# Performance work log

Measured on AMD Instinct MI355X. Metric: run time of the kernel, lower is better.

The kernel has to match this reference:

```python
import jax, jax.numpy as jnp
import numpy as np

B, N, DIM, H = 32, 480, 1024, 16


def setup_inputs() -> dict:
    key = jax.random.key(0)
    ks = jax.random.split(key, 7)
    s = 0.02
    return {
        "q": jax.random.normal(ks[0], (B, N, DIM), jnp.float32),
        "Wq": jax.random.normal(ks[1], (DIM, DIM), jnp.float32) * s,
        "Wk": jax.random.normal(ks[2], (DIM, DIM), jnp.float32) * s,
        "Wv": jax.random.normal(ks[3], (DIM, DIM), jnp.float32) * s,
        "pe": jax.random.normal(ks[4], (480, 480), jnp.float32),
        "Wo": jax.random.normal(ks[5], (DIM, DIM), jnp.float32) * s,
        "bo": jnp.zeros((DIM,), jnp.float32),
    }


def reference(q, Wq, Wk, Wv, pe, Wo, bo):
    b, n, dim = q.shape
    h = H
    d = dim // h
    scale = d ** -0.5
    # self-attention: k = v = q (pre-projection)
    qp = (q @ Wq.T).reshape(b, n, h, d).transpose(0, 2, 1, 3)  # b h n d
    kp = (q @ Wk.T).reshape(b, n, h, d).transpose(0, 2, 1, 3)
    vp = (q @ Wv.T).reshape(b, n, h, d).transpose(0, 2, 1, 3)
    dots = jnp.einsum("bhid,bhjd->bhij", qp, kp) * scale
    dots = dots + pe[:n, :n]  # learned additive positional bias
    attn = jax.nn.softmax(dots, axis=-1)
    out = jnp.einsum("bhij,bhjd->bhid", attn, vp)
    out = out.transpose(0, 2, 1, 3).reshape(b, n, dim)
    return out @ Wo.T + bo
```

## Files before the change

### kernel.cpp

```cpp
#include <hip/hip_runtime.h>
#include <hip/hip_bf16.h>
#include <stdint.h>

#define B_   32
#define N_   480
#define DIM_ 1024
#define H_   16
#define D_   64
#define M_   (B_*N_)
#define BH_  (B_*H_)

typedef __bf16 bf16;
typedef __bf16 bf16x4 __attribute__((ext_vector_type(4)));
typedef __bf16 bf16x8 __attribute__((ext_vector_type(8)));
typedef short  short4v __attribute__((ext_vector_type(4)));
typedef float  f32x4  __attribute__((ext_vector_type(4)));

__device__ __forceinline__ void gld_lds16(const void* g, void* l) {
    using GP = const __attribute__((address_space(1))) unsigned int*;
    using LP = __attribute__((address_space(3))) unsigned int*;
    __builtin_amdgcn_global_load_lds((GP)(uintptr_t)g, (LP)(unsigned int)(uintptr_t)l, 16, 0, 0);
}

__global__ void cvt4(const float* __restrict__ in, bf16* __restrict__ out, int n4) {
    int i = blockIdx.x * 256 + threadIdx.x;
    if (i >= n4) return;
    float4 v = ((const float4*)in)[i];
    bf16x4 o = { (bf16)v.x, (bf16)v.y, (bf16)v.z, (bf16)v.w };
    ((bf16x4*)out)[i] = o;
}

__global__ void cvtW(const float* __restrict__ Wq, const float* __restrict__ Wk,
                     const float* __restrict__ Wv, const float* __restrict__ Wo,
                     bf16* __restrict__ Wcat, bf16* __restrict__ Wob) {
    int i = blockIdx.x * 256 + threadIdx.x;
    const float* src; bf16* dst;
    switch (blockIdx.y) {
        case 0: src = Wq; dst = Wcat;                break;
        case 1: src = Wk; dst = Wcat + DIM_*DIM_;    break;
        case 2: src = Wv; dst = Wcat + 2*DIM_*DIM_;  break;
        default: src = Wo; dst = Wob;                break;
    }
    float4 v = ((const float4*)src)[i];
    bf16x4 o = { (bf16)v.x, (bf16)v.y, (bf16)v.z, (bf16)v.w };
    ((bf16x4*)dst)[i] = o;
}

#define GEMM_PRE()                                                            \
    const int tid  = threadIdx.x;                                             \
    const int lane = tid & 63;                                                \
    const int wid  = tid >> 6;                                                \
    const int wm   = wid & 1, wn = wid >> 1;                                  \
    const int m0   = blockIdx.y * 128;                                        \
    const int n0   = blockIdx.x * 128;                                        \
    const int lm   = lane & 15, lq = lane >> 4;                               \
    const int aLane = (lane >> 3) * 1024 + (((lane & 7) ^ (lane >> 3)) & 7) * 8; \
    const bf16* Asrc = A  + (m0 + wid*32) * 1024 + aLane;                     \
    const bf16* Bsrc = Bw + (n0 + wid*32) * 1024 + aLane;                     \
    bf16* AsDst = As + (wid*32)*64;                                           \
    bf16* BsDst = Bs + (wid*32)*64;                                           \
    int rowA[4], rowB[4];                                                     \
    _Pragma("unroll") for (int m = 0; m < 4; ++m) rowA[m] = (wm*64 + m*16 + lm)*64; \
    _Pragma("unroll") for (int n = 0; n < 4; ++n) rowB[n] = (wn*64 + n*16 + lm)*64; \
    const int sw = lm & 7;                                                    \
    int phys[2];                                                              \
    phys[0] = ((lq)     ^ sw) * 8;                                            \
    phys[1] = ((4 + lq) ^ sw) * 8;

#define GEMM_KLOOP(FIRST, SECOND)                                             \
    for (int k0 = 0; k0 < 1024; k0 += 64) {                                   \
        _Pragma("unroll") for (int j = 0; j < 4; ++j) {                       \
            gld_lds16(Asrc + k0 + j*8192, AsDst + j*512);                     \
            gld_lds16(Bsrc + k0 + j*8192, BsDst + j*512);                     \
        }                                                                     \
        __syncthreads();                                                      \
        _Pragma("unroll") for (int ks = 0; ks < 2; ++ks) {                    \
            bf16x8 af[4], bfr[4];                                             \
            _Pragma("unroll") for (int m = 0; m < 4; ++m)                     \
                af[m]  = *(const bf16x8*)&As[rowA[m] + phys[ks]];             \
            _Pragma("unroll") for (int n = 0; n < 4; ++n)                     \
                bfr[n] = *(const bf16x8*)&Bs[rowB[n] + phys[ks]];             \
            _Pragma("unroll") for (int m = 0; m < 4; ++m)                     \
                _Pragma("unroll") for (int n = 0; n < 4; ++n)                 \
                    acc[m][n] = __builtin_amdgcn_mfma_f32_16x16x32_bf16(      \
                        FIRST, SECOND, acc[m][n], 0, 0, 0);                   \
        }                                                                     \
        __syncthreads();                                                      \
    }

__global__ __launch_bounds__(256) void gemm_qkv(const bf16* __restrict__ A, const bf16* __restrict__ Bw,
                                                bf16* __restrict__ Qp, bf16* __restrict__ Kp,
                                                bf16* __restrict__ Vt) {
    __shared__ bf16 As[128*64];
    __shared__ bf16 Bs[128*64];
    GEMM_PRE();
    const int part = n0 >> 10;
    f32x4 acc[4][4] = {};

    if (part != 2) {
        GEMM_KLOOP(af[m], bfr[n]);
        bf16* dst = (part == 0) ? Qp : Kp;
        int hh[4], dd[4];
#pragma unroll
        for (int n = 0; n < 4; ++n) {
            int rem = (n0 + wn*64 + n*16 + lm) & 1023;
            hh[n] = rem >> 6; dd[n] = rem & 63;
        }
#pragma unroll
        for (int m = 0; m < 4; ++m) {
#pragma unroll
            for (int r = 0; r < 4; ++r) {
                int gm = m0 + wm*64 + m*16 + lq*4 + r;
                int b  = gm / 480;
                int nn = gm - b*480;
#pragma unroll
                for (int n = 0; n < 4; ++n)
                    dst[((b*16 + hh[n])*480 + nn)*64 + dd[n]] = (bf16)acc[m][n][r];
            }
        }
    } else {
        GEMM_KLOOP(bfr[n], af[m]);
#pragma unroll
        for (int m = 0; m < 4; ++m) {
            int gmBase = m0 + wm*64 + m*16;
            int b  = gmBase / 480;
            int nn = gmBase - b*480 + lm;
#pragma unroll
            for (int n = 0; n < 4; ++n)
#pragma unroll
                for (int r = 0; r < 4; ++r) {
                    int rem = (n0 + wn*64 + n*16 + lq*4 + r) & 1023;
                    int h = rem >> 6, d = rem & 63;
                    Vt[((b*16 + h)*64 + d)*480 + nn] = (bf16)acc[m][n][r];
                }
        }
    }
}

#define KT 96
#define KS_LD 72
#define VS_LD 104
__global__ __launch_bounds__(320) void attn(const bf16* __restrict__ Qp, const bf16* __restrict__ Kp,
                                            const bf16* __restrict__ Vt, const float* __restrict__ pe,
                                            bf16* __restrict__ O) {
    __shared__ bf16 Ks[KT*KS_LD];
    __shared__ bf16 Vs[64*VS_LD];
    const int tid  = threadIdx.x;
    const int lane = tid & 63, wid = tid >> 6;
    const int bh   = blockIdx.y;
    const int b    = bh >> 4, h = bh & 15;
    const int qblk = blockIdx.x * 80;
    const int lm   = lane & 15, lq = lane >> 4;
    const int qbase = bh * (N_ * 64);

    bf16x8 qb[2];
#pragma unroll
    for (int ks = 0; ks < 2; ++ks)
        qb[ks] = *(const bf16x8*)&Qp[qbase + (qblk + wid*16 + lm)*64 + ks*32 + lq*8];
    const float* peRow = pe + (qblk + wid*16 + lm)*480;

    f32x4 ot[4] = {};
    float lsum = 0.f;

    for (int kt = 0; kt < 5; ++kt) {
        __syncthreads();
        for (int c = tid; c < 768; c += 320) {
            int row = c >> 3, of = (c & 7) * 8;
            *(uint4*)&Ks[row*KS_LD + of] = *(const uint4*)&Kp[qbase + (kt*KT + row)*64 + of];
        }
        for (int c = tid; c < 768; c += 320) {
            int row = c / 12, of = (c % 12) * 8;
            *(uint4*)&Vs[row*VS_LD + of] = *(const uint4*)&Vt[qbase + row*480 + kt*KT + of];
        }
        __syncthreads();

        short4v pb[6];
#pragma unroll
        for (int mf = 0; mf < 6; ++mf) {
            f32x4 s = {};
#pragma unroll
            for (int ks = 0; ks < 2; ++ks) {
                bf16x8 ka = *(const bf16x8*)&Ks[(mf*16 + lm)*KS_LD + ks*32 + lq*8];
                s = __builtin_amdgcn_mfma_f32_16x16x32_bf16(ka, qb[ks], s, 0, 0, 0);
            }
            bf16x4 pv;
#pragma unroll
            for (int r = 0; r < 4; ++r) {
                float e = __expf(s[r] * 0.125f + peRow[kt*KT + mf*16 + lq*4 + r]);
                lsum += e;
                pv[r] = (bf16)e;
            }
            pb[mf] = __builtin_bit_cast(short4v, pv);
        }

#pragma unroll
        for (int df = 0; df < 4; ++df)
#pragma unroll
            for (int mf = 0; mf < 6; ++mf) {
                short4v va = *(const short4v*)&Vs[(df*16 + lm)*VS_LD + mf*16 + lq*4];
                ot[df] = __builtin_amdgcn_mfma_f32_16x16x16bf16_1k(va, pb[mf], ot[df], 0, 0, 0);
            }
    }

    lsum += __shfl_xor(lsum, 16);
    lsum += __shfl_xor(lsum, 32);
    float rl = 1.f / lsum;

    __syncthreads();
    bf16* Os = Ks;
#pragma unroll
    for (int df = 0; df < 4; ++df)
#pragma unroll
        for (int r = 0; r < 4; ++r)
            Os[(wid*16 + lm)*KS_LD + df*16 + lq*4 + r] = (bf16)(ot[df][r] * rl);
    __syncthreads();
    for (int c = tid; c < 640; c += 320) {
        int row = c >> 3, d0 = (c & 7) * 8;
        uint4 u = *(const uint4*)&Os[row*KS_LD + d0];
        *(uint4*)&O[(b*480 + qblk + row)*1024 + h*64 + d0] = u;
    }
}

__global__ __launch_bounds__(256) void gemm_out(const bf16* __restrict__ A, const bf16* __restrict__ Bw,
                                                const float* __restrict__ bo, float* __restrict__ out) {
    __shared__ bf16 As[128*64];
    __shared__ bf16 Bs[128*64];
    GEMM_PRE();
    f32x4 acc[4][4] = {};
    GEMM_KLOOP(af[m], bfr[n]);
#pragma unroll
    for (int m = 0; m < 4; ++m)
#pragma unroll
        for (int n = 0; n < 4; ++n)
#pragma unroll
            for (int r = 0; r < 4; ++r) {
                int gm = m0 + wm*64 + m*16 + lq*4 + r;
                int gn = n0 + wn*64 + n*16 + lm;
                out[gm*1024 + gn] = acc[m][n][r] + bo[gn];
            }
}

extern "C" void kernel_launch(void* const* d_in, const int* in_sizes, int n_in,
                              void* d_out, int out_size, void* d_ws, size_t ws_size,
                              hipStream_t stream) {
    const float* q  = (const float*)d_in[0];
    const float* Wq = (const float*)d_in[1];
    const float* Wk = (const float*)d_in[2];
    const float* Wv = (const float*)d_in[3];
    const float* pe = (const float*)d_in[4];
    const float* Wo = (const float*)d_in[5];
    const float* bo = (const float*)d_in[6];
    float* out = (float*)d_out;

    char* ws = (char*)d_ws;
    bf16* Abf  = (bf16*)(ws);
    bf16* Wcat = (bf16*)(ws + 31457280);
    bf16* Wob  = (bf16*)(ws + 31457280 + 6291456);
    bf16* Qp   = (bf16*)(ws + 39845888);
    bf16* Kp   = (bf16*)(ws + 71303168);
    bf16* Vt   = (bf16*)(ws + 102760448);

    cvt4<<<(M_*DIM_/4 + 255)/256, 256, 0, stream>>>(q, Abf, M_*DIM_/4);
    cvtW<<<dim3(DIM_*DIM_/4/256, 4), 256, 0, stream>>>(Wq, Wk, Wv, Wo, Wcat, Wob);

    gemm_qkv<<<dim3(24, 120), 256, 0, stream>>>(Abf, Wcat, Qp, Kp, Vt);
    attn<<<dim3(6, 512), 320, 0, stream>>>(Qp, Kp, Vt, pe, Abf);
    gemm_out<<<dim3(8, 120), 256, 0, stream>>>(Abf, Wob, bo, out);
}
```

Baseline: 414.1 us.

## Process two query tiles per wave in attention to reuse K/V LDS reads

Each wave in the attention kernel now handles 32 query rows as two 16-row tiles instead of one. Every K and V fragment read from LDS therefore feeds two MFMAs, and the block count along the query axis is halved. The LDS row pads also shrink and K/V share one buffer, and the output staging now uses vector stores. In exchange, register pressure roughly doubles for the accumulators, occupancy may drop, and the new pads leave rows only 8-byte aligned for the 16-byte LDS accesses.

Result: slower. 457.0 us (+10.4%).

```diff
diff --git a/kernel.cpp b/kernel.cpp
--- a/kernel.cpp
+++ b/kernel.cpp
@@ -138,29 +138,33 @@
 }
 
 #define KT 96
-#define KS_LD 72
-#define VS_LD 104
+#define KS_LD 68
+#define VS_LD 100
 __global__ __launch_bounds__(320) void attn(const bf16* __restrict__ Qp, const bf16* __restrict__ Kp,
                                             const bf16* __restrict__ Vt, const float* __restrict__ pe,
                                             bf16* __restrict__ O) {
-    __shared__ bf16 Ks[KT*KS_LD];
-    __shared__ bf16 Vs[64*VS_LD];
+    __shared__ bf16 Sm[KT*KS_LD + 64*VS_LD];
+    bf16* Ks = Sm;
+    bf16* Vs = Sm + KT*KS_LD;
     const int tid  = threadIdx.x;
     const int lane = tid & 63, wid = tid >> 6;
     const int bh   = blockIdx.y;
     const int b    = bh >> 4, h = bh & 15;
-    const int qblk = blockIdx.x * 80;
+    const int qblk = blockIdx.x * 160;
     const int lm   = lane & 15, lq = lane >> 4;
     const int qbase = bh * (N_ * 64);
 
-    bf16x8 qb[2];
-#pragma unroll
-    for (int ks = 0; ks < 2; ++ks)
-        qb[ks] = *(const bf16x8*)&Qp[qbase + (qblk + wid*16 + lm)*64 + ks*32 + lq*8];
-    const float* peRow = pe + (qblk + wid*16 + lm)*480;
-
-    f32x4 ot[4] = {};
-    float lsum = 0.f;
+    bf16x8 qb[2][2];
+#pragma unroll
+    for (int t = 0; t < 2; ++t)
+#pragma unroll
+        for (int ks = 0; ks < 2; ++ks)
+            qb[t][ks] = *(const bf16x8*)&Qp[qbase + (qblk + wid*32 + t*16 + lm)*64 + ks*32 + lq*8];
+    const float* peA = pe + (qblk + wid*32      + lm)*480;
+    const float* peB = pe + (qblk + wid*32 + 16 + lm)*480;
+
+    f32x4 ot[2][4] = {};
+    float lsum[2] = {0.f, 0.f};
 
     for (int kt = 0; kt < 5; ++kt) {
         __syncthreads();
@@ -174,23 +178,26 @@
         }
         __syncthreads();
 
-        short4v pb[6];
+        short4v pbA[6], pbB[6];
 #pragma unroll
         for (int mf = 0; mf < 6; ++mf) {
-            f32x4 s = {};
+            f32x4 sA = {}, sB = {};
 #pragma unroll
             for (int ks = 0; ks < 2; ++ks) {
                 bf16x8 ka = *(const bf16x8*)&Ks[(mf*16 + lm)*KS_LD + ks*32 + lq*8];
-                s = __builtin_amdgcn_mfma_f32_16x16x32_bf16(ka, qb[ks], s, 0, 0, 0);
-            }
-            bf16x4 pv;
+                sA = __builtin_amdgcn_mfma_f32_16x16x32_bf16(ka, qb[0][ks], sA, 0, 0, 0);
+                sB = __builtin_amdgcn_mfma_f32_16x16x32_bf16(ka, qb[1][ks], sB, 0, 0, 0);
+            }
+            bf16x4 pA, pB;
 #pragma unroll
             for (int r = 0; r < 4; ++r) {
-                float e = __expf(s[r] * 0.125f + peRow[kt*KT + mf*16 + lq*4 + r]);
-                lsum += e;
-                pv[r] = (bf16)e;
-            }
-            pb[mf] = __builtin_bit_cast(short4v, pv);
+                float eA = __expf(sA[r] * 0.125f + peA[kt*KT + mf*16 + lq*4 + r]);
+                float eB = __expf(sB[r] * 0.125f + peB[kt*KT + mf*16 + lq*4 + r]);
+                lsum[0] += eA; lsum[1] += eB;
+                pA[r] = (bf16)eA; pB[r] = (bf16)eB;
+            }
+            pbA[mf] = __builtin_bit_cast(short4v, pA);
+            pbB[mf] = __builtin_bit_cast(short4v, pB);
         }
 
 #pragma unroll
@@ -198,23 +205,32 @@
 #pragma unroll
             for (int mf = 0; mf < 6; ++mf) {
                 short4v va = *(const short4v*)&Vs[(df*16 + lm)*VS_LD + mf*16 + lq*4];
-                ot[df] = __builtin_amdgcn_mfma_f32_16x16x16bf16_1k(va, pb[mf], ot[df], 0, 0, 0);
-            }
-    }
-
-    lsum += __shfl_xor(lsum, 16);
-    lsum += __shfl_xor(lsum, 32);
-    float rl = 1.f / lsum;
+                ot[0][df] = __builtin_amdgcn_mfma_f32_16x16x16bf16_1k(va, pbA[mf], ot[0][df], 0, 0, 0);
+                ot[1][df] = __builtin_amdgcn_mfma_f32_16x16x16bf16_1k(va, pbB[mf], ot[1][df], 0, 0, 0);
+            }
+    }
+
+#pragma unroll
+    for (int t = 0; t < 2; ++t) {
+        lsum[t] += __shfl_xor(lsum[t], 16);
+        lsum[t] += __shfl_xor(lsum[t], 32);
+    }
 
     __syncthreads();
-    bf16* Os = Ks;
-#pragma unroll
-    for (int df = 0; df < 4; ++df)
-#pragma unroll
-        for (int r = 0; r < 4; ++r)
-            Os[(wid*16 + lm)*KS_LD + df*16 + lq*4 + r] = (bf16)(ot[df][r] * rl);
+    bf16* Os = Sm;
+#pragma unroll
+    for (int t = 0; t < 2; ++t) {
+        float rl = 1.f / lsum[t];
+#pragma unroll
+        for (int df = 0; df < 4; ++df) {
+            bf16x4 v;
+#pragma unroll
+            for (int r = 0; r < 4; ++r) v[r] = (bf16)(ot[t][df][r] * rl);
+            *(bf16x4*)&Os[(wid*32 + t*16 + lm)*KS_LD + df*16 + lq*4] = v;
+        }
+    }
     __syncthreads();
-    for (int c = tid; c < 640; c += 320) {
+    for (int c = tid; c < 1280; c += 320) {
         int row = c >> 3, d0 = (c & 7) * 8;
         uint4 u = *(const uint4*)&Os[row*KS_LD + d0];
         *(uint4*)&O[(b*480 + qblk + row)*1024 + h*64 + d0] = u;
@@ -264,6 +280,6 @@
     cvtW<<<dim3(DIM_*DIM_/4/256, 4), 256, 0, stream>>>(Wq, Wk, Wv, Wo, Wcat, Wob);
 
     gemm_qkv<<<dim3(24, 120), 256, 0, stream>>>(Abf, Wcat, Qp, Kp, Vt);
-    attn<<<dim3(6, 512), 320, 0, stream>>>(Qp, Kp, Vt, pe, Abf);
+    attn<<<dim3(3, 512), 320, 0, stream>>>(Qp, Kp, Vt, pe, Abf);
     gemm_out<<<dim3(8, 120), 256, 0, stream>>>(Abf, Wob, bo, out);
 }
```

## Prefetch K/V tiles into registers and widen attention blocks to six waves

Applied to the files above, without the earlier changes.

The attention kernel now loads the next K/V tile into registers while the current tile is being computed, instead of loading it from global memory right before each use. It also grows from 5 to 6 waves per block (96 query rows per block, 5 blocks per head). Other changes: the positional-bias reads and the output staging stores are vectorized, and the LDS row padding changes. The new paddings (68 and 100 elements) give row strides that are not multiples of 16 bytes, so the 128-bit LDS accesses may be misaligned, which could split them or break correctness.

New measurement: 457.8 us. 1.11x slower.

```diff
diff --git a/kernel.cpp b/kernel.cpp
--- a/kernel.cpp
+++ b/kernel.cpp
@@ -138,20 +138,26 @@
 }
 
 #define KT 96
-#define KS_LD 72
-#define VS_LD 104
-__global__ __launch_bounds__(320) void attn(const bf16* __restrict__ Qp, const bf16* __restrict__ Kp,
+#define KS_LD 68
+#define VS_LD 100
+__global__ __launch_bounds__(384) void attn(const bf16* __restrict__ Qp, const bf16* __restrict__ Kp,
                                             const bf16* __restrict__ Vt, const float* __restrict__ pe,
                                             bf16* __restrict__ O) {
-    __shared__ bf16 Ks[KT*KS_LD];
-    __shared__ bf16 Vs[64*VS_LD];
+    __shared__ bf16 Sm[KT*KS_LD + 64*VS_LD];
+    bf16* Ks = Sm;
+    bf16* Vs = Sm + KT*KS_LD;
     const int tid  = threadIdx.x;
     const int lane = tid & 63, wid = tid >> 6;
     const int bh   = blockIdx.y;
     const int b    = bh >> 4, h = bh & 15;
-    const int qblk = blockIdx.x * 80;
+    const int qblk = blockIdx.x * 96;
     const int lm   = lane & 15, lq = lane >> 4;
     const int qbase = bh * (N_ * 64);
+
+    const int kRow0 = tid >> 3,          kOff0 = (tid & 7) * 8;
+    const int kRow1 = (tid + 384) >> 3,  kOff1 = kOff0;
+    const int vRow0 = tid / 12,          vOff0 = (tid % 12) * 8;
+    const int vRow1 = (tid + 384) / 12,  vOff1 = ((tid + 384) % 12) * 8;
 
     bf16x8 qb[2];
 #pragma unroll
@@ -162,17 +168,28 @@
     f32x4 ot[4] = {};
     float lsum = 0.f;
 
+    uint4 kr0, kr1, vr0, vr1;
+    kr0 = *(const uint4*)&Kp[qbase + kRow0*64 + kOff0];
+    kr1 = *(const uint4*)&Kp[qbase + kRow1*64 + kOff1];
+    vr0 = *(const uint4*)&Vt[qbase + vRow0*480 + vOff0];
+    vr1 = *(const uint4*)&Vt[qbase + vRow1*480 + vOff1];
+
+#pragma unroll
     for (int kt = 0; kt < 5; ++kt) {
         __syncthreads();
-        for (int c = tid; c < 768; c += 320) {
-            int row = c >> 3, of = (c & 7) * 8;
-            *(uint4*)&Ks[row*KS_LD + of] = *(const uint4*)&Kp[qbase + (kt*KT + row)*64 + of];
-        }
-        for (int c = tid; c < 768; c += 320) {
-            int row = c / 12, of = (c % 12) * 8;
-            *(uint4*)&Vs[row*VS_LD + of] = *(const uint4*)&Vt[qbase + row*480 + kt*KT + of];
-        }
+        *(uint4*)&Ks[kRow0*KS_LD + kOff0] = kr0;
+        *(uint4*)&Ks[kRow1*KS_LD + kOff1] = kr1;
+        *(uint4*)&Vs[vRow0*VS_LD + vOff0] = vr0;
+        *(uint4*)&Vs[vRow1*VS_LD + vOff1] = vr1;
         __syncthreads();
+        if (kt < 4) {
+            int kb = qbase + (kt+1)*KT*64;
+            int vb = qbase + (kt+1)*KT;
+            kr0 = *(const uint4*)&Kp[kb + kRow0*64 + kOff0];
+            kr1 = *(const uint4*)&Kp[kb + kRow1*64 + kOff1];
+            vr0 = *(const uint4*)&Vt[vb + vRow0*480 + vOff0];
+            vr1 = *(const uint4*)&Vt[vb + vRow1*480 + vOff1];
+        }
 
         short4v pb[6];
 #pragma unroll
@@ -183,10 +200,11 @@
                 bf16x8 ka = *(const bf16x8*)&Ks[(mf*16 + lm)*KS_LD + ks*32 + lq*8];
                 s = __builtin_amdgcn_mfma_f32_16x16x32_bf16(ka, qb[ks], s, 0, 0, 0);
             }
+            f32x4 pv4 = *(const f32x4*)&peRow[kt*KT + mf*16 + lq*4];
             bf16x4 pv;
 #pragma unroll
             for (int r = 0; r < 4; ++r) {
-                float e = __expf(s[r] * 0.125f + peRow[kt*KT + mf*16 + lq*4 + r]);
+                float e = __expf(s[r] * 0.125f + pv4[r]);
                 lsum += e;
                 pv[r] = (bf16)e;
             }
@@ -207,14 +225,18 @@
     float rl = 1.f / lsum;
 
     __syncthreads();
-    bf16* Os = Ks;
-#pragma unroll
-    for (int df = 0; df < 4; ++df)
-#pragma unroll
-        for (int r = 0; r < 4; ++r)
-            Os[(wid*16 + lm)*KS_LD + df*16 + lq*4 + r] = (bf16)(ot[df][r] * rl);
+    bf16* Os = Sm;
+#pragma unroll
+    for (int df = 0; df < 4; ++df) {
+        bf16x4 v;
+#pragma unroll
+        for (int r = 0; r < 4; ++r) v[r] = (bf16)(ot[df][r] * rl);
+        *(bf16x4*)&Os[(wid*16 + lm)*KS_LD + df*16 + lq*4] = v;
+    }
     __syncthreads();
-    for (int c = tid; c < 640; c += 320) {
+#pragma unroll
+    for (int p = 0; p < 2; ++p) {
+        int c = p*384 + tid;
         int row = c >> 3, d0 = (c & 7) * 8;
         uint4 u = *(const uint4*)&Os[row*KS_LD + d0];
         *(uint4*)&O[(b*480 + qblk + row)*1024 + h*64 + d0] = u;
@@ -264,6 +286,6 @@
     cvtW<<<dim3(DIM_*DIM_/4/256, 4), 256, 0, stream>>>(Wq, Wk, Wv, Wo, Wcat, Wob);
 
     gemm_qkv<<<dim3(24, 120), 256, 0, stream>>>(Abf, Wcat, Qp, Kp, Vt);
-    attn<<<dim3(6, 512), 320, 0, stream>>>(Qp, Kp, Vt, pe, Abf);
+    attn<<<dim3(5, 512), 384, 0, stream>>>(Qp, Kp, Vt, pe, Abf);
     gemm_out<<<dim3(8, 120), 256, 0, stream>>>(Abf, Wob, bo, out);
 }
```
